# Kernel optimization log

Measured on AMD Instinct MI355X. Metric: run time of the kernel, lower is better.

The kernel has to match this reference:

```python
import jax, jax.numpy as jnp
import numpy as np

N_ITERS = 7
N_NODE_FEAT = 10   # GRU hidden size
N_NODE_IN = 9
N_EDGE_FEAT = 11
N_OUT = 2
MSG = 96


def setup_inputs() -> dict:
    key = jax.random.key(0)
    ks = jax.random.split(key, 20)
    N, E = 20000, 320000

    def lin(k, fan_in, fan_out):
        b = 1.0 / np.sqrt(fan_in)
        kw, kb = jax.random.split(k)
        W = jax.random.uniform(kw, (fan_out, fan_in), jnp.float32, -b, b)
        bias = jax.random.uniform(kb, (fan_out,), jnp.float32, -b, b)
        return W, bias

    W1, b1 = lin(ks[0], 2 * N_NODE_FEAT + N_EDGE_FEAT, MSG)
    W2, b2 = lin(ks[1], MSG, MSG)
    W3, b3 = lin(ks[2], MSG, MSG)
    W4, b4 = lin(ks[3], MSG, N_EDGE_FEAT)
    gru_in = N_EDGE_FEAT + N_NODE_IN
    gru_wih, gru_bih = lin(ks[4], gru_in, 3 * N_NODE_FEAT)
    gru_whh, gru_bhh = lin(ks[5], N_NODE_FEAT, 3 * N_NODE_FEAT)
    fin_w, fin_b = lin(ks[6], N_NODE_FEAT, N_OUT)

    return {
        'node_inputs': jax.random.normal(ks[7], (N, N_NODE_IN), jnp.float32),
        'edge_attr': jax.random.normal(ks[8], (E, N_EDGE_FEAT), jnp.float32),
        'W1': W1, 'b1': b1, 'W2': W2, 'b2': b2, 'W3': W3, 'b3': b3,
        'W4': W4, 'b4': b4,
        'gru_wih': gru_wih, 'gru_whh': gru_whh,
        'gru_bih': gru_bih, 'gru_bhh': gru_bhh,
        'fin_w': fin_w, 'fin_b': fin_b,
        'src_ids': jax.random.randint(ks[9], (E,), 0, N, jnp.int32),
        'dst_ids': jax.random.randint(ks[10], (E,), 0, N, jnp.int32),
    }


def reference(node_inputs, edge_attr, W1, b1, W2, b2, W3, b3, W4, b4,
              gru_wih, gru_whh, gru_bih, gru_bhh, fin_w, fin_b,
              src_ids, dst_ids):
    N = node_inputs.shape[0]
    H = gru_whh.shape[1]  # n_node_features

    def step(h, _):
        # edge MLP on gathered endpoint states  [E, 2H+F] -> [E, F]
        m = jnp.concatenate([h[src_ids], h[dst_ids], edge_attr], axis=1)
        m = jax.nn.relu(m @ W1.T + b1)
        m = jax.nn.relu(m @ W2.T + b2)
        m = jax.nn.relu(m @ W3.T + b3)
        msg = m @ W4.T + b4
        # scatter-add messages to destination nodes  [N, F]
        agg = jax.ops.segment_sum(msg, dst_ids, num_segments=N)
        # GRU cell (PyTorch gate order: r, z, n)
        x = jnp.concatenate([agg, node_inputs], axis=1)
        gi = x @ gru_wih.T + gru_bih
        gh = h @ gru_whh.T + gru_bhh
        i_r, i_z, i_n = jnp.split(gi, 3, axis=1)
        h_r, h_z, h_n = jnp.split(gh, 3, axis=1)
        r = jax.nn.sigmoid(i_r + h_r)
        z = jax.nn.sigmoid(i_z + h_z)
        n = jnp.tanh(i_n + r * h_n)
        h_new = (1.0 - z) * n + z * h
        logits = h_new @ fin_w.T + fin_b  # [N, 2]
        return h_new, logits

    h0 = jnp.zeros((N, H), node_inputs.dtype)
    _, outs = jax.lax.scan(step, h0, None, length=N_ITERS)
    return outs  # [T, N, 2]
```

## Files before the change

### kernel.cpp

```cpp
#include <hip/hip_runtime.h>
#include <math.h>
#include <stdint.h>

typedef _Float16 f16;
typedef f16 f16x8 __attribute__((ext_vector_type(8)));
typedef f16 f16x4 __attribute__((ext_vector_type(4)));
typedef float f32x4 __attribute__((ext_vector_type(4)));

#define N_ITERS 7
#define HF 10
#define NIN 9
#define EF 11
#define GIN (EF + NIN)

#define S1 40
#define S2 104
#define G  4
#define MSTR 12
#define RSTR 40

#define LPN 8

union FragU { f16x8 v; uint32_t u[4]; uint2 p2[2]; uint4 q4; };

__device__ __forceinline__ int sigmap(int k) {
    return 32 * (k >> 5) + 16 * ((k >> 2) & 1) + 4 * ((k >> 3) & 3) + (k & 3);
}

__global__ __launch_bounds__(256) void convert_and_count(
    const float* __restrict__ W1, const float* __restrict__ W2,
    const float* __restrict__ W3, const float* __restrict__ W4,
    f16* __restrict__ wf,
    const int* __restrict__ dst, int* __restrict__ cnt, int E)
{
    const int tid = blockIdx.x * 256 + threadIdx.x;
    const int nt = gridDim.x * 256;

    if (tid < E) atomicAdd(&cnt[dst[tid]], 1);

    f16* wf1 = wf;
    f16* wf2 = wf1 + 96 * S1;
    f16* wf3 = wf2 + 96 * S2;
    f16* wf4 = wf3 + 96 * S2;
    for (int i = tid; i < 96 * S1; i += nt) {
        int m = i / S1, k = i % S1;
        wf1[i] = (k < 31) ? (f16)W1[m * 31 + k] : (f16)0.f;
    }
    for (int i = tid; i < 96 * S2; i += nt) {
        int m = i / S2, k = i % S2;
        wf2[i] = (k < 96) ? (f16)W2[m * 96 + sigmap(k)] : (f16)0.f;
        wf3[i] = (k < 96) ? (f16)W3[m * 96 + sigmap(k)] : (f16)0.f;
    }
    for (int i = tid; i < 16 * S2; i += nt) {
        int m = i / S2, k = i % S2;
        wf4[i] = (m < 11 && k < 96) ? (f16)W4[m * 96 + sigmap(k)] : (f16)0.f;
    }
}

__global__ __launch_bounds__(1024) void scan_counts(
    const int* __restrict__ cnt, int* __restrict__ row_ptr,
    int* __restrict__ nxt, int N, int E)
{
    __shared__ int sums[1024];
    const int tid = threadIdx.x;
    const int C = (N + 1023) >> 10;
    const int base = tid * C;
    int local = 0;
    for (int i = 0; i < C; ++i) {
        int idx = base + i;
        if (idx < N) local += cnt[idx];
    }
    sums[tid] = local;
    __syncthreads();
    for (int off = 1; off < 1024; off <<= 1) {
        int v = (tid >= off) ? sums[tid - off] : 0;
        __syncthreads();
        sums[tid] += v;
        __syncthreads();
    }
    int run = sums[tid] - local;
    for (int i = 0; i < C; ++i) {
        int idx = base + i;
        if (idx < N) {
            row_ptr[idx] = run;
            nxt[idx] = run;
            run += cnt[idx];
        }
    }
    if (tid == 0) row_ptr[N] = E;
}

__global__ __launch_bounds__(256) void scatter_pack(
    const int* __restrict__ src, const int* __restrict__ dst,
    const float* __restrict__ ea, int* __restrict__ nxt,
    int* __restrict__ srcs, int* __restrict__ dsts,
    f16* __restrict__ eaA, f16* __restrict__ eaB, int E)
{
    int e = blockIdx.x * 256 + threadIdx.x;
    if (e >= E) return;
    const int d = dst[e];
    const int pos = atomicAdd(&nxt[d], 1);
    srcs[pos] = src[e];
    dsts[pos] = d;
    const float* r = ea + (size_t)e * EF;
    f16x4 a;
#pragma unroll
    for (int j = 0; j < 4; ++j) a[j] = (f16)r[j];
    *(f16x4*)(eaA + (size_t)pos * 4) = a;
    f16x8 b;
#pragma unroll
    for (int j = 0; j < 7; ++j) b[j] = (f16)r[4 + j];
    b[7] = (f16)0.f;
    *(f16x8*)(eaB + (size_t)pos * 8) = b;
}

__device__ __forceinline__ uint32_t pack_relu2(float x, float y) {
    union { f16 h[2]; uint32_t u; } r;
    r.h[0] = (f16)fmaxf(x, 0.0f);
    r.h[1] = (f16)fmaxf(y, 0.0f);
    return r.u;
}

#define MID_LAYER(WPTR, BPTR, IN, OUT)                                        \
    {                                                                         \
        _Pragma("unroll")                                                     \
        for (int t = 0; t < 6; ++t) {                                         \
            const f16x8 a0 = *(const f16x8*)(WPTR + (t * 16 + n) * S2 + 0 * 32 + 8 * q); \
            const f16x8 a1 = *(const f16x8*)(WPTR + (t * 16 + n) * S2 + 1 * 32 + 8 * q); \
            const f16x8 a2 = *(const f16x8*)(WPTR + (t * 16 + n) * S2 + 2 * 32 + 8 * q); \
            const f32x4 bias = *(const f32x4*)(BPTR + t * 16 + 4 * q);        \
            _Pragma("unroll")                                                 \
            for (int g = 0; g < G; ++g) {                                     \
                f32x4 c = bias;                                               \
                c = __builtin_amdgcn_mfma_f32_16x16x32_f16(a0, IN[g][0].v, c, 0, 0, 0); \
                c = __builtin_amdgcn_mfma_f32_16x16x32_f16(a1, IN[g][1].v, c, 0, 0, 0); \
                c = __builtin_amdgcn_mfma_f32_16x16x32_f16(a2, IN[g][2].v, c, 0, 0, 0); \
                OUT[g][t >> 1].u[2 * (t & 1) + 0] = pack_relu2(c[0], c[1]);   \
                OUT[g][t >> 1].u[2 * (t & 1) + 1] = pack_relu2(c[2], c[3]);   \
            }                                                                 \
        }                                                                     \
    }

__global__ __launch_bounds__(256, 2) void edge_mlp_mfma(
    const f16* __restrict__ h16, const f16* __restrict__ wf,
    const float* __restrict__ b1, const float* __restrict__ b2,
    const float* __restrict__ b3, const float* __restrict__ b4,
    const int* __restrict__ srcs, const int* __restrict__ dsts,
    const f16* __restrict__ eaA, const f16* __restrict__ eaB,
    float* __restrict__ msg, int E)
{
    const f16* wf1 = wf;
    const f16* wf2 = wf1 + 96 * S1;
    const f16* wf3 = wf2 + 96 * S2;
    const f16* wf4 = wf3 + 96 * S2;

    __shared__ f16 rec[256][RSTR];

    const int wave = threadIdx.x >> 6;
    const int lane = threadIdx.x & 63;
    const int n = lane & 15;
    const int q = lane >> 4;

    const int i0 = blockIdx.x * 256 + wave * (G * 16);

    {
        const int tid = threadIdx.x;
        const int i = blockIdx.x * 256 + tid;
        const int ii = (i < E) ? i : 0;
        const int s = srcs[ii];
        const int d = dsts[ii];
        const uint4* h16q = (const uint4*)h16;
        const uint32_t* h16u = (const uint32_t*)h16;
        uint4 hs0 = h16q[(size_t)s * 2];
        uint32_t hs1 = h16u[(size_t)s * 8 + 4];
        uint4 hd0 = h16q[(size_t)d * 2];
        uint32_t hd1 = h16u[(size_t)d * 8 + 4];
        uint2 ea0 = ((const uint2*)eaA)[ii];
        uint4 ea1 = ((const uint4*)eaB)[ii];
        uint4 w1 = { hs1, hd0.x, hd0.y, hd0.z };
        uint4 w2 = { hd0.w, hd1, ea0.x, ea0.y };
        uint4* rp = (uint4*)&rec[tid][0];
        rp[0] = hs0;
        rp[1] = w1;
        rp[2] = w2;
        rp[3] = ea1;
    }
    __syncthreads();

    FragU bfrA[G][3];
    FragU bfrB[G][3];

    {
        FragU bf[G];
#pragma unroll
        for (int g = 0; g < G; ++g)
            bf[g].v = *(const f16x8*)&rec[wave * 64 + g * 16 + n][q * 8];
#pragma unroll
        for (int t = 0; t < 6; ++t) {
            const f16x8 a = *(const f16x8*)(wf1 + (t * 16 + n) * S1 + 8 * q);
            const f32x4 bias = *(const f32x4*)(b1 + t * 16 + 4 * q);
#pragma unroll
            for (int g = 0; g < G; ++g) {
                f32x4 c = __builtin_amdgcn_mfma_f32_16x16x32_f16(a, bf[g].v, bias, 0, 0, 0);
                bfrA[g][t >> 1].u[2 * (t & 1) + 0] = pack_relu2(c[0], c[1]);
                bfrA[g][t >> 1].u[2 * (t & 1) + 1] = pack_relu2(c[2], c[3]);
            }
        }
    }

    MID_LAYER(wf2, b2, bfrA, bfrB)
    MID_LAYER(wf3, b3, bfrB, bfrA)

    {
        const f16x8 a0 = *(const f16x8*)(wf4 + n * S2 + 0 * 32 + 8 * q);
        const f16x8 a1 = *(const f16x8*)(wf4 + n * S2 + 1 * 32 + 8 * q);
        const f16x8 a2 = *(const f16x8*)(wf4 + n * S2 + 2 * 32 + 8 * q);
        float bias[4];
#pragma unroll
        for (int r = 0; r < 4; ++r) {
            const int m = 4 * q + r;
            bias[r] = (m < 11) ? b4[m] : 0.0f;
        }
#pragma unroll
        for (int g = 0; g < G; ++g) {
            f32x4 c = { bias[0], bias[1], bias[2], bias[3] };
            c = __builtin_amdgcn_mfma_f32_16x16x32_f16(a0, bfrA[g][0].v, c, 0, 0, 0);
            c = __builtin_amdgcn_mfma_f32_16x16x32_f16(a1, bfrA[g][1].v, c, 0, 0, 0);
            c = __builtin_amdgcn_mfma_f32_16x16x32_f16(a2, bfrA[g][2].v, c, 0, 0, 0);
            const int ig = i0 + g * 16 + n;
            if (q < 3 && ig < E)
                *(f32x4*)(msg + (size_t)ig * MSTR + 4 * q) = c;
        }
    }
}

__global__ __launch_bounds__(256) void gru_node_kernel(
    const float* __restrict__ node_inputs,
    float* __restrict__ h, f16* __restrict__ h16,
    const int* __restrict__ row_ptr, const float* __restrict__ msg,
    const float* __restrict__ wih, const float* __restrict__ whh,
    const float* __restrict__ bih, const float* __restrict__ bhh,
    const float* __restrict__ fw, const float* __restrict__ fb,
    float* __restrict__ out_t, int N)
{
    const int T = blockIdx.x * blockDim.x + threadIdx.x;
    const int n = T / LPN;
    const int sub = T & (LPN - 1);
    if (n >= N) return;

    float x[GIN];
#pragma unroll
    for (int k = 0; k < EF; ++k) x[k] = 0.0f;
    const int r0 = row_ptr[n], r1 = row_ptr[n + 1];
    for (int r = r0 + sub; r < r1; r += LPN) {
        const f32x4* mp = (const f32x4*)(msg + (size_t)r * MSTR);
        f32x4 a = mp[0], b = mp[1], c = mp[2];
        x[0] += a[0]; x[1] += a[1]; x[2] += a[2]; x[3] += a[3];
        x[4] += b[0]; x[5] += b[1]; x[6] += b[2]; x[7] += b[3];
        x[8] += c[0]; x[9] += c[1]; x[10] += c[2];
    }
#pragma unroll
    for (int off = 1; off < LPN; off <<= 1) {
#pragma unroll
        for (int k = 0; k < EF; ++k)
            x[k] += __shfl_xor(x[k], off);
    }
#pragma unroll
    for (int k = 0; k < NIN; ++k) x[EF + k] = node_inputs[(size_t)n * NIN + k];

    float hv[HF];
#pragma unroll
    for (int k = 0; k < HF; ++k) hv[k] = h[(size_t)n * HF + k];

    float hn[HF];
#pragma unroll
    for (int k = 0; k < HF; ++k) {
        float gir = bih[k];
        float giz = bih[HF + k];
        float gin = bih[2 * HF + k];
        float ghr = bhh[k];
        float ghz = bhh[HF + k];
        float ghn = bhh[2 * HF + k];
#pragma unroll
        for (int kk = 0; kk < GIN; ++kk) {
            gir = fmaf(x[kk], wih[(size_t)k * GIN + kk], gir);
            giz = fmaf(x[kk], wih[(size_t)(HF + k) * GIN + kk], giz);
            gin = fmaf(x[kk], wih[(size_t)(2 * HF + k) * GIN + kk], gin);
        }
#pragma unroll
        for (int kk = 0; kk < HF; ++kk) {
            ghr = fmaf(hv[kk], whh[(size_t)k * HF + kk], ghr);
            ghz = fmaf(hv[kk], whh[(size_t)(HF + k) * HF + kk], ghz);
            ghn = fmaf(hv[kk], whh[(size_t)(2 * HF + k) * HF + kk], ghn);
        }
        const float r2 = 1.0f / (1.0f + __expf(-(gir + ghr)));
        const float z  = 1.0f / (1.0f + __expf(-(giz + ghz)));
        const float nn = tanhf(gin + r2 * ghn);
        hn[k] = (1.0f - z) * nn + z * hv[k];
    }

    if (sub == 0) {
#pragma unroll
        for (int k = 0; k < HF; ++k) h[(size_t)n * HF + k] = hn[k];
        union { f16 hh[8]; uint4 q; } p4;
#pragma unroll
        for (int k = 0; k < 8; ++k) p4.hh[k] = (f16)hn[k];
        *(uint4*)(h16 + (size_t)n * 16) = p4.q;
        union { f16 hh[2]; uint32_t u; } p1;
        p1.hh[0] = (f16)hn[8]; p1.hh[1] = (f16)hn[9];
        *(uint32_t*)(h16 + (size_t)n * 16 + 8) = p1.u;

        float l0 = fb[0], l1 = fb[1];
#pragma unroll
        for (int k = 0; k < HF; ++k) {
            l0 = fmaf(hn[k], fw[k], l0);
            l1 = fmaf(hn[k], fw[HF + k], l1);
        }
        float2 lo = { l0, l1 };
        *(float2*)(out_t + (size_t)n * 2) = lo;
    }
}

extern "C" void kernel_launch(void* const* d_in, const int* in_sizes, int n_in,
                              void* d_out, int out_size, void* d_ws, size_t ws_size,
                              hipStream_t stream) {
    const float* node_inputs = (const float*)d_in[0];
    const float* edge_attr   = (const float*)d_in[1];
    const float* W1 = (const float*)d_in[2];
    const float* b1 = (const float*)d_in[3];
    const float* W2 = (const float*)d_in[4];
    const float* b2 = (const float*)d_in[5];
    const float* W3 = (const float*)d_in[6];
    const float* b3 = (const float*)d_in[7];
    const float* W4 = (const float*)d_in[8];
    const float* b4 = (const float*)d_in[9];
    const float* gru_wih = (const float*)d_in[10];
    const float* gru_whh = (const float*)d_in[11];
    const float* gru_bih = (const float*)d_in[12];
    const float* gru_bhh = (const float*)d_in[13];
    const float* fin_w   = (const float*)d_in[14];
    const float* fin_b   = (const float*)d_in[15];
    const int* src_ids = (const int*)d_in[16];
    const int* dst_ids = (const int*)d_in[17];

    const int N = in_sizes[0] / NIN;
    const int E = in_sizes[1] / EF;

    char* base = (char*)d_ws;
    size_t off = 0;
    auto alloc = [&](size_t bytes) -> char* {
        char* p = base + off;
        off += (bytes + 255) & ~(size_t)255;
        return p;
    };
    float* msg    = (float*)alloc((size_t)E * MSTR * 4);
    f16*   eaB    = (f16*)  alloc((size_t)E * 8 * 2);
    f16*   eaA    = (f16*)  alloc((size_t)E * 4 * 2);
    f16*   h16    = (f16*)  alloc((size_t)N * 16 * 2);
    float* hbuf   = (float*)alloc((size_t)N * HF * 4);
    int*   cnt    = (int*)  alloc((size_t)N * 4);
    f16*   wf     = (f16*)  alloc(52000 * 2);
    int*   row_ptr= (int*)  alloc((size_t)(N + 1) * 4);
    int*   nxt    = (int*)  alloc((size_t)N * 4);
    int*   srcs   = (int*)  alloc((size_t)E * 4);
    int*   dsts   = (int*)  alloc((size_t)E * 4);

    const int eb = (E + 255) / 256;
    const int nb = (N * LPN + 255) / 256;

    const size_t zspan = (size_t)((char*)cnt + (size_t)N * 4 - (char*)h16);
    hipMemsetAsync(h16, 0, zspan, stream);
    convert_and_count<<<eb, 256, 0, stream>>>(W1, W2, W3, W4, wf,
                                              dst_ids, cnt, E);
    scan_counts<<<1, 1024, 0, stream>>>(cnt, row_ptr, nxt, N, E);
    scatter_pack<<<eb, 256, 0, stream>>>(src_ids, dst_ids, edge_attr, nxt,
                                         srcs, dsts, eaA, eaB, E);

    float* out = (float*)d_out;
    for (int t = 0; t < N_ITERS; ++t) {
        edge_mlp_mfma<<<eb, 256, 0, stream>>>(
            h16, wf, b1, b2, b3, b4, srcs, dsts, eaA, eaB, msg, E);
        gru_node_kernel<<<nb, 256, 0, stream>>>(
            node_inputs, hbuf, h16, row_ptr, msg,
            gru_wih, gru_whh, gru_bih, gru_bhh,
            fin_w, fin_b, out + (size_t)t * N * 2, N);
    }
}
```

Baseline: 457.9 us.

## Persist edge MLP blocks over two tiles and prefetch next tile's gather

The edge MLP kernel now launches half as many blocks, and each block loops over tiles with a grid stride. While the MFMA layers run on the current tile, the kernel issues the gathers of node states and edge attributes for the next tile into registers, so global gather latency overlaps with compute. In exchange, the prefetched registers raise register pressure under launch_bounds(256,2), and the grid is halved, which may reduce occupancy and parallelism.

```diff
diff --git a/kernel.cpp b/kernel.cpp
--- a/kernel.cpp
+++ b/kernel.cpp
@@ -119,6 +119,28 @@
     r.h[0] = (f16)fmaxf(x, 0.0f);
     r.h[1] = (f16)fmaxf(y, 0.0f);
     return r.u;
+}
+
+struct GatherRegs { uint4 hs0; uint4 hd0; uint4 ea1; uint2 ea0; uint32_t hs1; uint32_t hd1; };
+
+__device__ __forceinline__ GatherRegs gather_edge(
+    const f16* __restrict__ h16, const int* __restrict__ srcs,
+    const int* __restrict__ dsts, const f16* __restrict__ eaA,
+    const f16* __restrict__ eaB, int i, int E)
+{
+    const int ii = (i < E) ? i : 0;
+    const int s = srcs[ii];
+    const int d = dsts[ii];
+    const uint4* h16q = (const uint4*)h16;
+    const uint32_t* h16u = (const uint32_t*)h16;
+    GatherRegs g;
+    g.hs0 = h16q[(size_t)s * 2];
+    g.hs1 = h16u[(size_t)s * 8 + 4];
+    g.hd0 = h16q[(size_t)d * 2];
+    g.hd1 = h16u[(size_t)d * 8 + 4];
+    g.ea0 = ((const uint2*)eaA)[ii];
+    g.ea1 = ((const uint4*)eaB)[ii];
+    return g;
 }
 
 #define MID_LAYER(WPTR, BPTR, IN, OUT)                                        \
@@ -156,81 +178,85 @@
 
     __shared__ f16 rec[256][RSTR];
 
-    const int wave = threadIdx.x >> 6;
-    const int lane = threadIdx.x & 63;
+    const int tid = threadIdx.x;
+    const int wave = tid >> 6;
+    const int lane = tid & 63;
     const int n = lane & 15;
     const int q = lane >> 4;
-
-    const int i0 = blockIdx.x * 256 + wave * (G * 16);
-
-    {
-        const int tid = threadIdx.x;
-        const int i = blockIdx.x * 256 + tid;
-        const int ii = (i < E) ? i : 0;
-        const int s = srcs[ii];
-        const int d = dsts[ii];
-        const uint4* h16q = (const uint4*)h16;
-        const uint32_t* h16u = (const uint32_t*)h16;
-        uint4 hs0 = h16q[(size_t)s * 2];
-        uint32_t hs1 = h16u[(size_t)s * 8 + 4];
-        uint4 hd0 = h16q[(size_t)d * 2];
-        uint32_t hd1 = h16u[(size_t)d * 8 + 4];
-        uint2 ea0 = ((const uint2*)eaA)[ii];
-        uint4 ea1 = ((const uint4*)eaB)[ii];
-        uint4 w1 = { hs1, hd0.x, hd0.y, hd0.z };
-        uint4 w2 = { hd0.w, hd1, ea0.x, ea0.y };
-        uint4* rp = (uint4*)&rec[tid][0];
-        rp[0] = hs0;
-        rp[1] = w1;
-        rp[2] = w2;
-        rp[3] = ea1;
-    }
-    __syncthreads();
-
-    FragU bfrA[G][3];
-    FragU bfrB[G][3];
-
-    {
-        FragU bf[G];
-#pragma unroll
-        for (int g = 0; g < G; ++g)
-            bf[g].v = *(const f16x8*)&rec[wave * 64 + g * 16 + n][q * 8];
-#pragma unroll
-        for (int t = 0; t < 6; ++t) {
-            const f16x8 a = *(const f16x8*)(wf1 + (t * 16 + n) * S1 + 8 * q);
-            const f32x4 bias = *(const f32x4*)(b1 + t * 16 + 4 * q);
+    const int nTiles = (E + 255) >> 8;
+
+    int tile = blockIdx.x;
+    GatherRegs gr = gather_edge(h16, srcs, dsts, eaA, eaB, tile * 256 + tid, E);
+
+    for (;;) {
+        __syncthreads();
+        {
+            uint4 w1 = { gr.hs1, gr.hd0.x, gr.hd0.y, gr.hd0.z };
+            uint4 w2 = { gr.hd0.w, gr.hd1, gr.ea0.x, gr.ea0.y };
+            uint4* rp = (uint4*)&rec[tid][0];
+            rp[0] = gr.hs0;
+            rp[1] = w1;
+            rp[2] = w2;
+            rp[3] = gr.ea1;
+        }
+        __syncthreads();
+
+        const int next = tile + gridDim.x;
+        const bool more = next < nTiles;
+        const int gidx = (more ? next : tile) * 256 + tid;
+        GatherRegs grn = gather_edge(h16, srcs, dsts, eaA, eaB, gidx, E);
+
+        const int i0 = tile * 256 + wave * (G * 16);
+
+        FragU bfrA[G][3];
+        FragU bfrB[G][3];
+
+        {
+            FragU bf[G];
+#pragma unroll
+            for (int g = 0; g < G; ++g)
+                bf[g].v = *(const f16x8*)&rec[wave * 64 + g * 16 + n][q * 8];
+#pragma unroll
+            for (int t = 0; t < 6; ++t) {
+                const f16x8 a = *(const f16x8*)(wf1 + (t * 16 + n) * S1 + 8 * q);
+                const f32x4 bias = *(const f32x4*)(b1 + t * 16 + 4 * q);
+#pragma unroll
+                for (int g = 0; g < G; ++g) {
+                    f32x4 c = __builtin_amdgcn_mfma_f32_16x16x32_f16(a, bf[g].v, bias, 0, 0, 0);
+                    bfrA[g][t >> 1].u[2 * (t & 1) + 0] = pack_relu2(c[0], c[1]);
+                    bfrA[g][t >> 1].u[2 * (t & 1) + 1] = pack_relu2(c[2], c[3]);
+                }
+            }
+        }
+
+        MID_LAYER(wf2, b2, bfrA, bfrB)
+        MID_LAYER(wf3, b3, bfrB, bfrA)
+
+        {
+            const f16x8 a0 = *(const f16x8*)(wf4 + n * S2 + 0 * 32 + 8 * q);
+            const f16x8 a1 = *(const f16x8*)(wf4 + n * S2 + 1 * 32 + 8 * q);
+            const f16x8 a2 = *(const f16x8*)(wf4 + n * S2 + 2 * 32 + 8 * q);
+            float bias[4];
+#pragma unroll
+            for (int r = 0; r < 4; ++r) {
+                const int m = 4 * q + r;
+                bias[r] = (m < 11) ? b4[m] : 0.0f;
+            }
 #pragma unroll
             for (int g = 0; g < G; ++g) {
-                f32x4 c = __builtin_amdgcn_mfma_f32_16x16x32_f16(a, bf[g].v, bias, 0, 0, 0);
-                bfrA[g][t >> 1].u[2 * (t & 1) + 0] = pack_relu2(c[0], c[1]);
-                bfrA[g][t >> 1].u[2 * (t & 1) + 1] = pack_relu2(c[2], c[3]);
+                f32x4 c = { bias[0], bias[1], bias[2], bias[3] };
+                c = __builtin_amdgcn_mfma_f32_16x16x32_f16(a0, bfrA[g][0].v, c, 0, 0, 0);
+                c = __builtin_amdgcn_mfma_f32_16x16x32_f16(a1, bfrA[g][1].v, c, 0, 0, 0);
+                c = __builtin_amdgcn_mfma_f32_16x16x32_f16(a2, bfrA[g][2].v, c, 0, 0, 0);
+                const int ig = i0 + g * 16 + n;
+                if (q < 3 && ig < E)
+                    *(f32x4*)(msg + (size_t)ig * MSTR + 4 * q) = c;
             }
         }
-    }
-
-    MID_LAYER(wf2, b2, bfrA, bfrB)
-    MID_LAYER(wf3, b3, bfrB, bfrA)
-
-    {
-        const f16x8 a0 = *(const f16x8*)(wf4 + n * S2 + 0 * 32 + 8 * q);
-        const f16x8 a1 = *(const f16x8*)(wf4 + n * S2 + 1 * 32 + 8 * q);
-        const f16x8 a2 = *(const f16x8*)(wf4 + n * S2 + 2 * 32 + 8 * q);
-        float bias[4];
-#pragma unroll
-        for (int r = 0; r < 4; ++r) {
-            const int m = 4 * q + r;
-            bias[r] = (m < 11) ? b4[m] : 0.0f;
-        }
-#pragma unroll
-        for (int g = 0; g < G; ++g) {
-            f32x4 c = { bias[0], bias[1], bias[2], bias[3] };
-            c = __builtin_amdgcn_mfma_f32_16x16x32_f16(a0, bfrA[g][0].v, c, 0, 0, 0);
-            c = __builtin_amdgcn_mfma_f32_16x16x32_f16(a1, bfrA[g][1].v, c, 0, 0, 0);
-            c = __builtin_amdgcn_mfma_f32_16x16x32_f16(a2, bfrA[g][2].v, c, 0, 0, 0);
-            const int ig = i0 + g * 16 + n;
-            if (q < 3 && ig < E)
-                *(f32x4*)(msg + (size_t)ig * MSTR + 4 * q) = c;
-        }
+
+        if (!more) break;
+        gr = grn;
+        tile = next;
     }
 }
 
@@ -366,6 +392,7 @@
     int*   dsts   = (int*)  alloc((size_t)E * 4);
 
     const int eb = (E + 255) / 256;
+    const int eb2 = (eb + 1) / 2;
     const int nb = (N * LPN + 255) / 256;
 
     const size_t zspan = (size_t)((char*)cnt + (size_t)N * 4 - (char*)h16);
@@ -378,7 +405,7 @@
 
     float* out = (float*)d_out;
     for (int t = 0; t < N_ITERS; ++t) {
-        edge_mlp_mfma<<<eb, 256, 0, stream>>>(
+        edge_mlp_mfma<<<eb2, 256, 0, stream>>>(
             h16, wf, b1, b2, b3, b4, srcs, dsts, eaA, eaB, msg, E);
         gru_node_kernel<<<nb, 256, 0, stream>>>(
             node_inputs, hbuf, h16, row_ptr, msg,
```

Result: slower. 943.9 us (+106.2%).
